# Optimization experiments

Hardware: AMD Instinct MI355X
Metric: run time of the kernel (lower is better)

The kernel has to match this reference:

```python
import jax, jax.numpy as jnp
import numpy as np

NUM_HEADS = 16
BLOCK_SIZE = 512


def setup_inputs() -> dict:
    key = jax.random.key(0)
    ks = jax.random.split(key, 5)
    B, S, D = 2, 4096, 1024
    scale = 1.0 / np.sqrt(D)
    return {
        "x": jax.random.normal(ks[0], (B, S, D), dtype=jnp.float32),
        "w_q": jax.random.normal(ks[1], (D, D), dtype=jnp.float32) * scale,
        "w_k": jax.random.normal(ks[2], (D, D), dtype=jnp.float32) * scale,
        "w_v": jax.random.normal(ks[3], (D, D), dtype=jnp.float32) * scale,
        "w_o": jax.random.normal(ks[4], (D, D), dtype=jnp.float32) * scale,
    }


def _ring_attention(q, k, v, block_size):
    # q,k,v: [B, H, S, Dh]; online-softmax accumulation over KV blocks
    B, H, S, Dh = q.shape
    scale = 1.0 / np.sqrt(Dh).astype(np.float32)
    nb = S // block_size
    # [nb, B, H, block, Dh] so lax.scan iterates over KV blocks
    kb = k.reshape(B, H, nb, block_size, Dh).transpose(2, 0, 1, 3, 4)
    vb = v.reshape(B, H, nb, block_size, Dh).transpose(2, 0, 1, 3, 4)

    m0 = jnp.full((B, H, S), -jnp.inf, dtype=q.dtype)
    l0 = jnp.zeros((B, H, S), dtype=q.dtype)
    o0 = jnp.zeros((B, H, S, Dh), dtype=q.dtype)

    def step(carry, kv):
        m, l, o = carry
        kj, vj = kv                                   # [B,H,block,Dh]
        s = jnp.einsum("bhqd,bhkd->bhqk", q, kj) * scale  # [B,H,S,block]
        m_new = jnp.maximum(m, s.max(axis=-1))
        alpha = jnp.exp(m - m_new)                    # rescale old stats
        p = jnp.exp(s - m_new[..., None])             # unnormalized probs
        o = o * alpha[..., None] + jnp.einsum("bhqk,bhkd->bhqd", p, vj)
        l = l * alpha + p.sum(axis=-1)
        return (m_new, l, o), None

    (m, l, o), _ = jax.lax.scan(step, (m0, l0, o0), (kb, vb))
    return o / l[..., None]


def reference(x, w_q, w_k, w_v, w_o):
    B, S, D = x.shape
    H = NUM_HEADS
    Dh = D // H
    q = (x @ w_q).reshape(B, S, H, Dh).transpose(0, 2, 1, 3)
    k = (x @ w_k).reshape(B, S, H, Dh).transpose(0, 2, 1, 3)
    v = (x @ w_v).reshape(B, S, H, Dh).transpose(0, 2, 1, 3)
    out = _ring_attention(q, k, v, BLOCK_SIZE)        # [B,H,S,Dh]
    out = out.transpose(0, 2, 1, 3).reshape(B, S, D)
    return out @ w_o
```

## Files before the change

### kernel.cpp

```cpp
#include <hip/hip_runtime.h>
#include <stdint.h>

#define B_ 2
#define S_ 4096
#define D_ 1024
#define H_ 16
#define DH_ 64
#define M_ 8192

typedef __attribute__((ext_vector_type(8))) short short8;
typedef __attribute__((ext_vector_type(4))) float f32x4;
typedef __attribute__((ext_vector_type(16))) float f32x16;
typedef __attribute__((ext_vector_type(2))) unsigned int uint2v;
typedef __attribute__((ext_vector_type(4))) unsigned int uint4v;

__device__ __forceinline__ unsigned short f2bf(float f) {
  union { float f; unsigned int u; } v; v.f = f;
  return (unsigned short)((v.u + 0x7FFFu + ((v.u >> 16) & 1u)) >> 16);
}

__device__ __forceinline__ unsigned int cvtpk_bf16(float lo, float hi) {
  unsigned int r;
  asm("v_cvt_pk_bf16_f32 %0, %1, %2" : "=v"(r) : "v"(lo), "v"(hi));
  return r;
}

__device__ __forceinline__ void gld_lds16(const void* g, void* l) {
  __builtin_amdgcn_global_load_lds(
      (const __attribute__((address_space(1))) void*)g,
      (__attribute__((address_space(3))) void*)l, 16, 0, 0);
}

__global__ void conv_x(const float* __restrict__ X, unsigned short* __restrict__ Xb) {
  size_t i = ((size_t)blockIdx.x * 256 + threadIdx.x) * 8;
  float4 a = *(const float4*)(X + i);
  float4 b = *(const float4*)(X + i + 4);
  uint4 pk;
  pk.x = (unsigned int)f2bf(a.x) | ((unsigned int)f2bf(a.y) << 16);
  pk.y = (unsigned int)f2bf(a.z) | ((unsigned int)f2bf(a.w) << 16);
  pk.z = (unsigned int)f2bf(b.x) | ((unsigned int)f2bf(b.y) << 16);
  pk.w = (unsigned int)f2bf(b.z) | ((unsigned int)f2bf(b.w) << 16);
  *(uint4*)(Xb + i) = pk;
}

__global__ __launch_bounds__(256)
void conv_w(const float* __restrict__ W0, const float* __restrict__ W1,
            const float* __restrict__ W2, const float* __restrict__ W3,
            unsigned short* __restrict__ T0, unsigned short* __restrict__ T1,
            unsigned short* __restrict__ T2, unsigned short* __restrict__ T3) {
  __shared__ float tile[64][65];
  const int z = blockIdx.z;
  const float* W = (z == 0) ? W0 : (z == 1) ? W1 : (z == 2) ? W2 : W3;
  unsigned short* T = (z == 0) ? T0 : (z == 1) ? T1 : (z == 2) ? T2 : T3;
  const int k0 = blockIdx.x * 64, n0 = blockIdx.y * 64;
  const int t = threadIdx.x;
  const int r = t >> 2;
  const int c = (t & 3) * 16;

  const float* src = W + (size_t)(k0 + r) * D_ + n0 + c;
  float4 a0 = *(const float4*)(src + 0);
  float4 a1 = *(const float4*)(src + 4);
  float4 a2 = *(const float4*)(src + 8);
  float4 a3 = *(const float4*)(src + 12);
  tile[r][c + 0] = a0.x;  tile[r][c + 1] = a0.y;  tile[r][c + 2] = a0.z;  tile[r][c + 3] = a0.w;
  tile[r][c + 4] = a1.x;  tile[r][c + 5] = a1.y;  tile[r][c + 6] = a1.z;  tile[r][c + 7] = a1.w;
  tile[r][c + 8] = a2.x;  tile[r][c + 9] = a2.y;  tile[r][c + 10] = a2.z; tile[r][c + 11] = a2.w;
  tile[r][c + 12] = a3.x; tile[r][c + 13] = a3.y; tile[r][c + 14] = a3.z; tile[r][c + 15] = a3.w;
  __syncthreads();

  unsigned int pk[8];
  #pragma unroll
  for (int i = 0; i < 8; ++i) {
    unsigned short lo = f2bf(tile[c + 2 * i + 0][r]);
    unsigned short hi = f2bf(tile[c + 2 * i + 1][r]);
    pk[i] = (unsigned int)lo | ((unsigned int)hi << 16);
  }
  unsigned short* dst = T + (size_t)(n0 + r) * D_ + k0 + c;
  *(uint4*)(dst + 0) = *(uint4*)&pk[0];
  *(uint4*)(dst + 8) = *(uint4*)&pk[4];
}

__global__ __launch_bounds__(256, 2)
void gemm_qkv(const unsigned short* __restrict__ Xb,
              const unsigned short* __restrict__ Wq,
              const unsigned short* __restrict__ Wk,
              const unsigned short* __restrict__ Wv,
              unsigned short* __restrict__ Qb,
              unsigned short* __restrict__ Kb,
              unsigned short* __restrict__ Vtb) {
  __shared__ char As[16384];
  __shared__ char Bs[16384];
  const int tid = threadIdx.x, wave = tid >> 6, lane = tid & 63;
  const int lg = lane >> 4, ll = lane & 15;
  const int m0 = blockIdx.x * 128, n0 = blockIdx.y * 128, z = blockIdx.z;
  const unsigned short* Wt = (z == 0) ? Wq : ((z == 1) ? Wk : Wv);
  const int wr = wave >> 1, wc = wave & 1;
  f32x4 acc[4][4];
  #pragma unroll
  for (int a = 0; a < 4; ++a)
    #pragma unroll
    for (int b = 0; b < 4; ++b) acc[a][b] = (f32x4){0.f, 0.f, 0.f, 0.f};

  const char* Ag = (const char*)Xb;
  const char* Bg = (const char*)Wt;
  for (int kt = 0; kt < 16; ++kt) {
    __syncthreads();
    #pragma unroll
    for (int i = 0; i < 2; ++i) {
      int s0 = wave * 256 + i * 128 + lane;
      int row0 = s0 >> 3, colb0 = (s0 & 7) * 16;
      gld_lds16(Ag + (size_t)(m0 + row0) * 2048 + kt * 128 + colb0, As + wave * 4096 + i * 2048);
      gld_lds16(Bg + (size_t)(n0 + row0) * 2048 + kt * 128 + colb0, Bs + wave * 4096 + i * 2048);
      int s1 = s0 + 64;
      int row1 = s1 >> 3, colb1 = (s1 & 7) * 16;
      gld_lds16(Ag + (size_t)(m0 + row1) * 2048 + kt * 128 + colb1, As + wave * 4096 + i * 2048 + 1024);
      gld_lds16(Bg + (size_t)(n0 + row1) * 2048 + kt * 128 + colb1, Bs + wave * 4096 + i * 2048 + 1024);
    }
    __syncthreads();
    #pragma unroll
    for (int c = 0; c < 2; ++c) {
      short8 af[4], bf[4];
      #pragma unroll
      for (int i = 0; i < 4; ++i) {
        af[i] = *(const short8*)(As + (wr * 64 + i * 16 + ll) * 128 + lg * 16 + c * 64);
        bf[i] = *(const short8*)(Bs + (wc * 64 + i * 16 + ll) * 128 + lg * 16 + c * 64);
      }
      #pragma unroll
      for (int mi = 0; mi < 4; ++mi)
        #pragma unroll
        for (int ni = 0; ni < 4; ++ni)
          acc[mi][ni] = __builtin_amdgcn_mfma_f32_16x16x32_bf16(af[mi], bf[ni], acc[mi][ni], 0, 0, 0);
    }
  }

  if (z == 0) {
    const float sc = 0.18033688011112042f;
    #pragma unroll
    for (int mi = 0; mi < 4; ++mi)
      #pragma unroll
      for (int ni = 0; ni < 4; ++ni)
        #pragma unroll
        for (int j = 0; j < 4; ++j) {
          int m = m0 + wr * 64 + mi * 16 + lg * 4 + j;
          int n = n0 + wc * 64 + ni * 16 + ll;
          int bh = (m >> 12) * H_ + (n >> 6);
          Qb[((size_t)bh * S_ + (m & 4095)) * DH_ + (n & 63)] = f2bf(acc[mi][ni][j] * sc);
        }
  } else if (z == 1) {
    #pragma unroll
    for (int mi = 0; mi < 4; ++mi)
      #pragma unroll
      for (int ni = 0; ni < 4; ++ni)
        #pragma unroll
        for (int j = 0; j < 4; ++j) {
          int m = m0 + wr * 64 + mi * 16 + lg * 4 + j;
          int n = n0 + wc * 64 + ni * 16 + ll;
          int s = m & 4095, d = n & 63;
          int bh = (m >> 12) * H_ + (n >> 6);
          size_t off = (size_t)bh * 262144 + (size_t)(s >> 5) * 2048 +
                       (size_t)(d >> 4) * 512 + (size_t)((d >> 3) & 1) * 256 +
                       (size_t)(s & 31) * 8 + (d & 7);
          Kb[off] = f2bf(acc[mi][ni][j]);
        }
  } else {
    #pragma unroll
    for (int mi = 0; mi < 4; ++mi)
      #pragma unroll
      for (int ni = 0; ni < 4; ++ni) {
        int mb = m0 + wr * 64 + mi * 16 + lg * 4;
        int n = n0 + wc * 64 + ni * 16 + ll;
        int s0 = mb & 4095, d = n & 63;
        int bh = (mb >> 12) * H_ + (n >> 6);
        size_t off = (size_t)bh * 262144 + (size_t)(s0 >> 5) * 2048 +
                     (size_t)((s0 >> 4) & 1) * 1024 + (size_t)(d >> 5) * 512 +
                     (size_t)((s0 >> 3) & 1) * 256 + (size_t)(d & 31) * 8 + (s0 & 7);
        uint2 pk;
        pk.x = (unsigned int)f2bf(acc[mi][ni][0]) | ((unsigned int)f2bf(acc[mi][ni][1]) << 16);
        pk.y = (unsigned int)f2bf(acc[mi][ni][2]) | ((unsigned int)f2bf(acc[mi][ni][3]) << 16);
        *(uint2*)(Vtb + off) = pk;
      }
  }
}

__global__ __launch_bounds__(64, 2)
void attn_kernel(const unsigned short* __restrict__ Qb,
                 const unsigned short* __restrict__ Kf,
                 const unsigned short* __restrict__ Vf,
                 unsigned short* __restrict__ Ob) {
  const int lane = threadIdx.x & 63;
  const int hh = lane >> 5;
  const int ql = lane & 31;

  const int hw = blockIdx.x;
  const int virt = (hw & 7) * 256 + (hw >> 3);
  const int bh = virt >> 6, qblk = virt & 63;
  const int qbase = qblk * 64;

  const char* Qg = (const char*)Qb + (size_t)bh * S_ * 128;
  short8 qa[4], qb2[4];
  #pragma unroll
  for (int c = 0; c < 4; ++c) {
    qa[c]  = *(const short8*)(Qg + (size_t)(qbase + ql) * 128 + c * 32 + hh * 16);
    qb2[c] = *(const short8*)(Qg + (size_t)(qbase + 32 + ql) * 128 + c * 32 + hh * 16);
  }

  f32x16 oa0, oa1, ob0, ob1, zf;
  #pragma unroll
  for (int i = 0; i < 16; ++i) { oa0[i] = 0.f; oa1[i] = 0.f; ob0[i] = 0.f; ob1[i] = 0.f; zf[i] = 0.f; }
  float la = 0.f, lb = 0.f;

  const char* Kg = (const char*)Kf + (size_t)bh * 524288 + lane * 16;
  const char* Vg = (const char*)Vf + (size_t)bh * 524288 + lane * 16;

#define LOADK(dst, t) do { const char* p_ = Kg + (size_t)(t) * 4096; \
    dst[0] = *(const short8*)(p_); dst[1] = *(const short8*)(p_ + 1024); \
    dst[2] = *(const short8*)(p_ + 2048); dst[3] = *(const short8*)(p_ + 3072); } while (0)
#define LOADV(dst, t) do { const char* p_ = Vg + (size_t)(t) * 4096; \
    dst[0] = *(const short8*)(p_); dst[1] = *(const short8*)(p_ + 1024); \
    dst[2] = *(const short8*)(p_ + 2048); dst[3] = *(const short8*)(p_ + 3072); } while (0)

  short8 kA[4], vA[4], kB[4], vB[4];
  LOADK(kA, 0); LOADV(vA, 0);
  LOADK(kB, 1); LOADV(vB, 1);

#define ITER(KR, VR, TP, PF) do { \
    f32x16 pa, pb; \
    __builtin_amdgcn_s_setprio(1); \
    pa = __builtin_amdgcn_mfma_f32_32x32x16_bf16(KR[0], qa[0], zf, 0, 0, 0); \
    pb = __builtin_amdgcn_mfma_f32_32x32x16_bf16(KR[0], qb2[0], zf, 0, 0, 0); \
    pa = __builtin_amdgcn_mfma_f32_32x32x16_bf16(KR[1], qa[1], pa, 0, 0, 0); \
    pb = __builtin_amdgcn_mfma_f32_32x32x16_bf16(KR[1], qb2[1], pb, 0, 0, 0); \
    pa = __builtin_amdgcn_mfma_f32_32x32x16_bf16(KR[2], qa[2], pa, 0, 0, 0); \
    pb = __builtin_amdgcn_mfma_f32_32x32x16_bf16(KR[2], qb2[2], pb, 0, 0, 0); \
    pa = __builtin_amdgcn_mfma_f32_32x32x16_bf16(KR[3], qa[3], pa, 0, 0, 0); \
    pb = __builtin_amdgcn_mfma_f32_32x32x16_bf16(KR[3], qb2[3], pb, 0, 0, 0); \
    __builtin_amdgcn_s_setprio(0); \
    if (PF) { LOADK(KR, TP); } \
    _Pragma("unroll") \
    for (int i = 0; i < 16; ++i) pa[i] = __builtin_amdgcn_exp2f(pa[i]); \
    uint4v pqa0, pqa1; \
    { \
      uint2v r; \
      r = __builtin_amdgcn_permlane32_swap(cvtpk_bf16(pa[0], pa[1]), cvtpk_bf16(pa[4], pa[5]), false, false); \
      pqa0.x = r[0]; pqa0.z = r[1]; \
      r = __builtin_amdgcn_permlane32_swap(cvtpk_bf16(pa[2], pa[3]), cvtpk_bf16(pa[6], pa[7]), false, false); \
      pqa0.y = r[0]; pqa0.w = r[1]; \
      r = __builtin_amdgcn_permlane32_swap(cvtpk_bf16(pa[8], pa[9]), cvtpk_bf16(pa[12], pa[13]), false, false); \
      pqa1.x = r[0]; pqa1.z = r[1]; \
      r = __builtin_amdgcn_permlane32_swap(cvtpk_bf16(pa[10], pa[11]), cvtpk_bf16(pa[14], pa[15]), false, false); \
      pqa1.y = r[0]; pqa1.w = r[1]; \
    } \
    _Pragma("unroll") \
    for (int i = 0; i < 16; ++i) pb[i] = __builtin_amdgcn_exp2f(pb[i]); \
    uint4v pqb0, pqb1; \
    { \
      uint2v r; \
      r = __builtin_amdgcn_permlane32_swap(cvtpk_bf16(pb[0], pb[1]), cvtpk_bf16(pb[4], pb[5]), false, false); \
      pqb0.x = r[0]; pqb0.z = r[1]; \
      r = __builtin_amdgcn_permlane32_swap(cvtpk_bf16(pb[2], pb[3]), cvtpk_bf16(pb[6], pb[7]), false, false); \
      pqb0.y = r[0]; pqb0.w = r[1]; \
      r = __builtin_amdgcn_permlane32_swap(cvtpk_bf16(pb[8], pb[9]), cvtpk_bf16(pb[12], pb[13]), false, false); \
      pqb1.x = r[0]; pqb1.z = r[1]; \
      r = __builtin_amdgcn_permlane32_swap(cvtpk_bf16(pb[10], pb[11]), cvtpk_bf16(pb[14], pb[15]), false, false); \
      pqb1.y = r[0]; pqb1.w = r[1]; \
    } \
    __builtin_amdgcn_s_setprio(1); \
    { \
      short8 psa = __builtin_bit_cast(short8, pqa0); \
      short8 psb = __builtin_bit_cast(short8, pqb0); \
      oa0 = __builtin_amdgcn_mfma_f32_32x32x16_bf16(VR[0], psa, oa0, 0, 0, 0); \
      oa1 = __builtin_amdgcn_mfma_f32_32x32x16_bf16(VR[1], psa, oa1, 0, 0, 0); \
      ob0 = __builtin_amdgcn_mfma_f32_32x32x16_bf16(VR[0], psb, ob0, 0, 0, 0); \
      ob1 = __builtin_amdgcn_mfma_f32_32x32x16_bf16(VR[1], psb, ob1, 0, 0, 0); \
    } \
    { \
      short8 psa = __builtin_bit_cast(short8, pqa1); \
      short8 psb = __builtin_bit_cast(short8, pqb1); \
      oa0 = __builtin_amdgcn_mfma_f32_32x32x16_bf16(VR[2], psa, oa0, 0, 0, 0); \
      oa1 = __builtin_amdgcn_mfma_f32_32x32x16_bf16(VR[3], psa, oa1, 0, 0, 0); \
      ob0 = __builtin_amdgcn_mfma_f32_32x32x16_bf16(VR[2], psb, ob0, 0, 0, 0); \
      ob1 = __builtin_amdgcn_mfma_f32_32x32x16_bf16(VR[3], psb, ob1, 0, 0, 0); \
    } \
    __builtin_amdgcn_s_setprio(0); \
    if (PF) { LOADV(VR, TP); } \
    float s0_ = ((pa[0] + pa[1]) + (pa[2] + pa[3])) + ((pa[4] + pa[5]) + (pa[6] + pa[7])); \
    float s1_ = ((pa[8] + pa[9]) + (pa[10] + pa[11])) + ((pa[12] + pa[13]) + (pa[14] + pa[15])); \
    float s2_ = ((pb[0] + pb[1]) + (pb[2] + pb[3])) + ((pb[4] + pb[5]) + (pb[6] + pb[7])); \
    float s3_ = ((pb[8] + pb[9]) + (pb[10] + pb[11])) + ((pb[12] + pb[13]) + (pb[14] + pb[15])); \
    float ra_ = s0_ + s1_, rb_ = s2_ + s3_; \
    ra_ += __shfl_xor(ra_, 32); \
    rb_ += __shfl_xor(rb_, 32); \
    la += ra_; lb += rb_; \
  } while (0)

  for (int t = 0; t < 128; t += 2) {
    ITER(kA, vA, t + 2, (t + 2 < 128));
    ITER(kB, vB, t + 3, (t + 3 < 128));
  }

  float inva = 1.f / la, invb = 1.f / lb;
  unsigned short* OpA = Ob + ((size_t)(bh >> 4) * S_ + qbase + ql) * D_ + (bh & 15) * DH_;
  unsigned short* OpB = Ob + ((size_t)(bh >> 4) * S_ + qbase + 32 + ql) * D_ + (bh & 15) * DH_;
  #pragma unroll
  for (int g = 0; g < 4; ++g) {
    uint2 pk2;
    pk2.x = (unsigned int)f2bf(oa0[4 * g + 0] * inva) | ((unsigned int)f2bf(oa0[4 * g + 1] * inva) << 16);
    pk2.y = (unsigned int)f2bf(oa0[4 * g + 2] * inva) | ((unsigned int)f2bf(oa0[4 * g + 3] * inva) << 16);
    *(uint2*)(OpA + g * 8 + hh * 4) = pk2;
    pk2.x = (unsigned int)f2bf(oa1[4 * g + 0] * inva) | ((unsigned int)f2bf(oa1[4 * g + 1] * inva) << 16);
    pk2.y = (unsigned int)f2bf(oa1[4 * g + 2] * inva) | ((unsigned int)f2bf(oa1[4 * g + 3] * inva) << 16);
    *(uint2*)(OpA + 32 + g * 8 + hh * 4) = pk2;
    pk2.x = (unsigned int)f2bf(ob0[4 * g + 0] * invb) | ((unsigned int)f2bf(ob0[4 * g + 1] * invb) << 16);
    pk2.y = (unsigned int)f2bf(ob0[4 * g + 2] * invb) | ((unsigned int)f2bf(ob0[4 * g + 3] * invb) << 16);
    *(uint2*)(OpB + g * 8 + hh * 4) = pk2;
    pk2.x = (unsigned int)f2bf(ob1[4 * g + 0] * invb) | ((unsigned int)f2bf(ob1[4 * g + 1] * invb) << 16);
    pk2.y = (unsigned int)f2bf(ob1[4 * g + 2] * invb) | ((unsigned int)f2bf(ob1[4 * g + 3] * invb) << 16);
    *(uint2*)(OpB + 32 + g * 8 + hh * 4) = pk2;
  }
#undef LOADK
#undef LOADV
#undef ITER
}

__global__ __launch_bounds__(256, 2)
void gemm_o(const unsigned short* __restrict__ Ab,
            const unsigned short* __restrict__ Wo,
            float* __restrict__ Out) {
  __shared__ char As[16384];
  __shared__ char Bs[16384];
  const int tid = threadIdx.x, wave = tid >> 6, lane = tid & 63;
  const int lg = lane >> 4, ll = lane & 15;
  const int m0 = blockIdx.x * 128, n0 = blockIdx.y * 128;
  const int wr = wave >> 1, wc = wave & 1;
  f32x4 acc[4][4];
  #pragma unroll
  for (int a = 0; a < 4; ++a)
    #pragma unroll
    for (int b = 0; b < 4; ++b) acc[a][b] = (f32x4){0.f, 0.f, 0.f, 0.f};

  const char* Ag = (const char*)Ab;
  const char* Bg = (const char*)Wo;
  for (int kt = 0; kt < 16; ++kt) {
    __syncthreads();
    #pragma unroll
    for (int i = 0; i < 4; ++i) {
      int s = wave * 256 + i * 64 + lane;
      int row = s >> 3, colb = (s & 7) * 16;
      gld_lds16(Ag + (size_t)(m0 + row) * 2048 + kt * 128 + colb, As + wave * 4096 + i * 1024);
      gld_lds16(Bg + (size_t)(n0 + row) * 2048 + kt * 128 + colb, Bs + wave * 4096 + i * 1024);
    }
    __syncthreads();
    #pragma unroll
    for (int c = 0; c < 2; ++c) {
      short8 af[4], bf[4];
      #pragma unroll
      for (int i = 0; i < 4; ++i) {
        af[i] = *(const short8*)(As + (wr * 64 + i * 16 + ll) * 128 + lg * 16 + c * 64);
        bf[i] = *(const short8*)(Bs + (wc * 64 + i * 16 + ll) * 128 + lg * 16 + c * 64);
      }
      #pragma unroll
      for (int mi = 0; mi < 4; ++mi)
        #pragma unroll
        for (int ni = 0; ni < 4; ++ni)
          acc[mi][ni] = __builtin_amdgcn_mfma_f32_16x16x32_bf16(af[mi], bf[ni], acc[mi][ni], 0, 0, 0);
    }
  }
  #pragma unroll
  for (int mi = 0; mi < 4; ++mi)
    #pragma unroll
    for (int ni = 0; ni < 4; ++ni)
      #pragma unroll
      for (int j = 0; j < 4; ++j) {
        int m = m0 + wr * 64 + mi * 16 + lg * 4 + j;
        int n = n0 + wc * 64 + ni * 16 + ll;
        Out[(size_t)m * D_ + n] = acc[mi][ni][j];
      }
}

extern "C" void kernel_launch(void* const* d_in, const int* in_sizes, int n_in,
                              void* d_out, int out_size, void* d_ws, size_t ws_size,
                              hipStream_t stream) {
  const float* x  = (const float*)d_in[0];
  const float* wq = (const float*)d_in[1];
  const float* wk = (const float*)d_in[2];
  const float* wv = (const float*)d_in[3];
  const float* wo = (const float*)d_in[4];
  float* out = (float*)d_out;
  char* ws = (char*)d_ws;

  unsigned short* Xb = (unsigned short*)(ws);
  unsigned short* Wq = (unsigned short*)(ws + (16u << 20));
  unsigned short* Wk = (unsigned short*)(ws + (18u << 20));
  unsigned short* Wv = (unsigned short*)(ws + (20u << 20));
  unsigned short* Wo = (unsigned short*)(ws + (22u << 20));
  unsigned short* Qb = (unsigned short*)(ws + (24u << 20));
  unsigned short* Kb = (unsigned short*)(ws + (40u << 20));
  unsigned short* Vt = (unsigned short*)(ws + (56u << 20));
  unsigned short* Ob = (unsigned short*)(ws + (72u << 20));

  conv_x<<<dim3(4096), dim3(256), 0, stream>>>(x, Xb);
  conv_w<<<dim3(16, 16, 4), dim3(256), 0, stream>>>(wq, wk, wv, wo, Wq, Wk, Wv, Wo);
  gemm_qkv<<<dim3(64, 8, 3), dim3(256), 0, stream>>>(Xb, Wq, Wk, Wv, Qb, Kb, Vt);
  attn_kernel<<<dim3(2048), dim3(64), 0, stream>>>(Qb, Kb, Vt, Ob);
  gemm_o<<<dim3(64, 8), dim3(256), 0, stream>>>(Ob, Wo, out);
}
```

Before: 255.3 us.

## Use 32x32x16 MFMA with XOR-swizzled LDS tiles in projection GEMMs

Both the QKV and output projection GEMMs switch from 16x16x32 to 32x32x16 bf16 MFMA tiles, with 2x2 f32x16 accumulators per wave. The global-to-LDS loads now XOR-swizzle the 16-byte column chunks by row, and the fragment reads apply the matching XOR. The goal is fewer LDS reads per MFMA and fewer bank conflicts on the fragment loads. The epilogue index mapping is rewritten for the 32x32 accumulator layout, which risks layout mistakes in the Q/K/V scatter stores.

New measurement: 248.4 us. -2.7%, faster.

```diff
diff --git a/kernel.cpp b/kernel.cpp
--- a/kernel.cpp
+++ b/kernel.cpp
@@ -91,94 +91,98 @@
   __shared__ char As[16384];
   __shared__ char Bs[16384];
   const int tid = threadIdx.x, wave = tid >> 6, lane = tid & 63;
-  const int lg = lane >> 4, ll = lane & 15;
+  const int hh = lane >> 5, l31 = lane & 31;
   const int m0 = blockIdx.x * 128, n0 = blockIdx.y * 128, z = blockIdx.z;
   const unsigned short* Wt = (z == 0) ? Wq : ((z == 1) ? Wk : Wv);
   const int wr = wave >> 1, wc = wave & 1;
-  f32x4 acc[4][4];
-  #pragma unroll
-  for (int a = 0; a < 4; ++a)
-    #pragma unroll
-    for (int b = 0; b < 4; ++b) acc[a][b] = (f32x4){0.f, 0.f, 0.f, 0.f};
+  f32x16 acc[2][2];
+  #pragma unroll
+  for (int a = 0; a < 2; ++a)
+    #pragma unroll
+    for (int b = 0; b < 2; ++b)
+      #pragma unroll
+      for (int i = 0; i < 16; ++i) acc[a][b][i] = 0.f;
 
   const char* Ag = (const char*)Xb;
   const char* Bg = (const char*)Wt;
+  const int sw = (((lane & 7) ^ (lane >> 3)) << 4);
+  const int xa = (l31 & 7) << 4;
+
   for (int kt = 0; kt < 16; ++kt) {
     __syncthreads();
     #pragma unroll
-    for (int i = 0; i < 2; ++i) {
-      int s0 = wave * 256 + i * 128 + lane;
-      int row0 = s0 >> 3, colb0 = (s0 & 7) * 16;
-      gld_lds16(Ag + (size_t)(m0 + row0) * 2048 + kt * 128 + colb0, As + wave * 4096 + i * 2048);
-      gld_lds16(Bg + (size_t)(n0 + row0) * 2048 + kt * 128 + colb0, Bs + wave * 4096 + i * 2048);
-      int s1 = s0 + 64;
-      int row1 = s1 >> 3, colb1 = (s1 & 7) * 16;
-      gld_lds16(Ag + (size_t)(m0 + row1) * 2048 + kt * 128 + colb1, As + wave * 4096 + i * 2048 + 1024);
-      gld_lds16(Bg + (size_t)(n0 + row1) * 2048 + kt * 128 + colb1, Bs + wave * 4096 + i * 2048 + 1024);
+    for (int i = 0; i < 4; ++i) {
+      int row = wave * 32 + i * 8 + (lane >> 3);
+      gld_lds16(Ag + (size_t)(m0 + row) * 2048 + kt * 128 + sw, As + wave * 4096 + i * 1024);
+      gld_lds16(Bg + (size_t)(n0 + row) * 2048 + kt * 128 + sw, Bs + wave * 4096 + i * 1024);
     }
     __syncthreads();
     #pragma unroll
-    for (int c = 0; c < 2; ++c) {
-      short8 af[4], bf[4];
-      #pragma unroll
-      for (int i = 0; i < 4; ++i) {
-        af[i] = *(const short8*)(As + (wr * 64 + i * 16 + ll) * 128 + lg * 16 + c * 64);
-        bf[i] = *(const short8*)(Bs + (wc * 64 + i * 16 + ll) * 128 + lg * 16 + c * 64);
+    for (int ks = 0; ks < 4; ++ks) {
+      short8 af[2], bf[2];
+      #pragma unroll
+      for (int i = 0; i < 2; ++i) {
+        int ra = wr * 64 + i * 32 + l31;
+        af[i] = *(const short8*)(As + ra * 128 + ((ks * 32 + hh * 16) ^ xa));
+        int rb = wc * 64 + i * 32 + l31;
+        bf[i] = *(const short8*)(Bs + rb * 128 + ((ks * 32 + hh * 16) ^ xa));
       }
       #pragma unroll
-      for (int mi = 0; mi < 4; ++mi)
+      for (int mi = 0; mi < 2; ++mi)
         #pragma unroll
-        for (int ni = 0; ni < 4; ++ni)
-          acc[mi][ni] = __builtin_amdgcn_mfma_f32_16x16x32_bf16(af[mi], bf[ni], acc[mi][ni], 0, 0, 0);
+        for (int ni = 0; ni < 2; ++ni)
+          acc[mi][ni] = __builtin_amdgcn_mfma_f32_32x32x16_bf16(af[mi], bf[ni], acc[mi][ni], 0, 0, 0);
     }
   }
 
   if (z == 0) {
     const float sc = 0.18033688011112042f;
     #pragma unroll
-    for (int mi = 0; mi < 4; ++mi)
-      #pragma unroll
-      for (int ni = 0; ni < 4; ++ni)
+    for (int mi = 0; mi < 2; ++mi)
+      #pragma unroll
+      for (int ni = 0; ni < 2; ++ni)
         #pragma unroll
-        for (int j = 0; j < 4; ++j) {
-          int m = m0 + wr * 64 + mi * 16 + lg * 4 + j;
-          int n = n0 + wc * 64 + ni * 16 + ll;
+        for (int r = 0; r < 16; ++r) {
+          int m = m0 + wr * 64 + mi * 32 + (r & 3) + 8 * (r >> 2) + 4 * hh;
+          int n = n0 + wc * 64 + ni * 32 + l31;
           int bh = (m >> 12) * H_ + (n >> 6);
-          Qb[((size_t)bh * S_ + (m & 4095)) * DH_ + (n & 63)] = f2bf(acc[mi][ni][j] * sc);
+          Qb[((size_t)bh * S_ + (m & 4095)) * DH_ + (n & 63)] = f2bf(acc[mi][ni][r] * sc);
         }
   } else if (z == 1) {
     #pragma unroll
-    for (int mi = 0; mi < 4; ++mi)
-      #pragma unroll
-      for (int ni = 0; ni < 4; ++ni)
+    for (int mi = 0; mi < 2; ++mi)
+      #pragma unroll
+      for (int ni = 0; ni < 2; ++ni)
         #pragma unroll
-        for (int j = 0; j < 4; ++j) {
-          int m = m0 + wr * 64 + mi * 16 + lg * 4 + j;
-          int n = n0 + wc * 64 + ni * 16 + ll;
+        for (int r = 0; r < 16; ++r) {
+          int m = m0 + wr * 64 + mi * 32 + (r & 3) + 8 * (r >> 2) + 4 * hh;
+          int n = n0 + wc * 64 + ni * 32 + l31;
           int s = m & 4095, d = n & 63;
           int bh = (m >> 12) * H_ + (n >> 6);
           size_t off = (size_t)bh * 262144 + (size_t)(s >> 5) * 2048 +
                        (size_t)(d >> 4) * 512 + (size_t)((d >> 3) & 1) * 256 +
                        (size_t)(s & 31) * 8 + (d & 7);
-          Kb[off] = f2bf(acc[mi][ni][j]);
+          Kb[off] = f2bf(acc[mi][ni][r]);
         }
   } else {
     #pragma unroll
-    for (int mi = 0; mi < 4; ++mi)
-      #pragma unroll
-      for (int ni = 0; ni < 4; ++ni) {
-        int mb = m0 + wr * 64 + mi * 16 + lg * 4;
-        int n = n0 + wc * 64 + ni * 16 + ll;
-        int s0 = mb & 4095, d = n & 63;
-        int bh = (mb >> 12) * H_ + (n >> 6);
-        size_t off = (size_t)bh * 262144 + (size_t)(s0 >> 5) * 2048 +
-                     (size_t)((s0 >> 4) & 1) * 1024 + (size_t)(d >> 5) * 512 +
-                     (size_t)((s0 >> 3) & 1) * 256 + (size_t)(d & 31) * 8 + (s0 & 7);
-        uint2 pk;
-        pk.x = (unsigned int)f2bf(acc[mi][ni][0]) | ((unsigned int)f2bf(acc[mi][ni][1]) << 16);
-        pk.y = (unsigned int)f2bf(acc[mi][ni][2]) | ((unsigned int)f2bf(acc[mi][ni][3]) << 16);
-        *(uint2*)(Vtb + off) = pk;
-      }
+    for (int mi = 0; mi < 2; ++mi)
+      #pragma unroll
+      for (int ni = 0; ni < 2; ++ni)
+        #pragma unroll
+        for (int g = 0; g < 4; ++g) {
+          int mb = m0 + wr * 64 + mi * 32 + 8 * g + 4 * hh;
+          int n = n0 + wc * 64 + ni * 32 + l31;
+          int s0 = mb & 4095, d = n & 63;
+          int bh = (mb >> 12) * H_ + (n >> 6);
+          size_t off = (size_t)bh * 262144 + (size_t)(s0 >> 5) * 2048 +
+                       (size_t)((s0 >> 4) & 1) * 1024 + (size_t)(d >> 5) * 512 +
+                       (size_t)((s0 >> 3) & 1) * 256 + (size_t)(d & 31) * 8 + (s0 & 7);
+          uint2 pk;
+          pk.x = (unsigned int)f2bf(acc[mi][ni][4 * g + 0]) | ((unsigned int)f2bf(acc[mi][ni][4 * g + 1]) << 16);
+          pk.y = (unsigned int)f2bf(acc[mi][ni][4 * g + 2]) | ((unsigned int)f2bf(acc[mi][ni][4 * g + 3]) << 16);
+          *(uint2*)(Vtb + off) = pk;
+        }
   }
 }
 
@@ -329,51 +333,57 @@
   __shared__ char As[16384];
   __shared__ char Bs[16384];
   const int tid = threadIdx.x, wave = tid >> 6, lane = tid & 63;
-  const int lg = lane >> 4, ll = lane & 15;
+  const int hh = lane >> 5, l31 = lane & 31;
   const int m0 = blockIdx.x * 128, n0 = blockIdx.y * 128;
   const int wr = wave >> 1, wc = wave & 1;
-  f32x4 acc[4][4];
-  #pragma unroll
-  for (int a = 0; a < 4; ++a)
-    #pragma unroll
-    for (int b = 0; b < 4; ++b) acc[a][b] = (f32x4){0.f, 0.f, 0.f, 0.f};
+  f32x16 acc[2][2];
+  #pragma unroll
+  for (int a = 0; a < 2; ++a)
+    #pragma unroll
+    for (int b = 0; b < 2; ++b)
+      #pragma unroll
+      for (int i = 0; i < 16; ++i) acc[a][b][i] = 0.f;
 
   const char* Ag = (const char*)Ab;
   const char* Bg = (const char*)Wo;
+  const int sw = (((lane & 7) ^ (lane >> 3)) << 4);
+  const int xa = (l31 & 7) << 4;
+
   for (int kt = 0; kt < 16; ++kt) {
     __syncthreads();
     #pragma unroll
     for (int i = 0; i < 4; ++i) {
-      int s = wave * 256 + i * 64 + lane;
-      int row = s >> 3, colb = (s & 7) * 16;
-      gld_lds16(Ag + (size_t)(m0 + row) * 2048 + kt * 128 + colb, As + wave * 4096 + i * 1024);
-      gld_lds16(Bg + (size_t)(n0 + row) * 2048 + kt * 128 + colb, Bs + wave * 4096 + i * 1024);
+      int row = wave * 32 + i * 8 + (lane >> 3);
+      gld_lds16(Ag + (size_t)(m0 + row) * 2048 + kt * 128 + sw, As + wave * 4096 + i * 1024);
+      gld_lds16(Bg + (size_t)(n0 + row) * 2048 + kt * 128 + sw, Bs + wave * 4096 + i * 1024);
     }
     __syncthreads();
     #pragma unroll
-    for (int c = 0; c < 2; ++c) {
-      short8 af[4], bf[4];
-      #pragma unroll
-      for (int i = 0; i < 4; ++i) {
-        af[i] = *(const short8*)(As + (wr * 64 + i * 16 + ll) * 128 + lg * 16 + c * 64);
-        bf[i] = *(const short8*)(Bs + (wc * 64 + i * 16 + ll) * 128 + lg * 16 + c * 64);
+    for (int ks = 0; ks < 4; ++ks) {
+      short8 af[2], bf[2];
+      #pragma unroll
+      for (int i = 0; i < 2; ++i) {
+        int ra = wr * 64 + i * 32 + l31;
+        af[i] = *(const short8*)(As + ra * 128 + ((ks * 32 + hh * 16) ^ xa));
+        int rb = wc * 64 + i * 32 + l31;
+        bf[i] = *(const short8*)(Bs + rb * 128 + ((ks * 32 + hh * 16) ^ xa));
       }
       #pragma unroll
-      for (int mi = 0; mi < 4; ++mi)
+      for (int mi = 0; mi < 2; ++mi)
         #pragma unroll
-        for (int ni = 0; ni < 4; ++ni)
-          acc[mi][ni] = __builtin_amdgcn_mfma_f32_16x16x32_bf16(af[mi], bf[ni], acc[mi][ni], 0, 0, 0);
+        for (int ni = 0; ni < 2; ++ni)
+          acc[mi][ni] = __builtin_amdgcn_mfma_f32_32x32x16_bf16(af[mi], bf[ni], acc[mi][ni], 0, 0, 0);
     }
   }
   #pragma unroll
-  for (int mi = 0; mi < 4; ++mi)
-    #pragma unroll
-    for (int ni = 0; ni < 4; ++ni)
-      #pragma unroll
-      for (int j = 0; j < 4; ++j) {
-        int m = m0 + wr * 64 + mi * 16 + lg * 4 + j;
-        int n = n0 + wc * 64 + ni * 16 + ll;
-        Out[(size_t)m * D_ + n] = acc[mi][ni][j];
+  for (int mi = 0; mi < 2; ++mi)
+    #pragma unroll
+    for (int ni = 0; ni < 2; ++ni)
+      #pragma unroll
+      for (int r = 0; r < 16; ++r) {
+        int m = m0 + wr * 64 + mi * 32 + (r & 3) + 8 * (r >> 2) + 4 * hh;
+        int n = n0 + wc * 64 + ni * 32 + l31;
+        Out[(size_t)m * D_ + n] = acc[mi][ni][r];
       }
 }
 
```
